# Performance work log

Measured on AMD Instinct MI355X. Metric: run time of the kernel, lower is better.

Reference implementation:

```python
import jax, jax.numpy as jnp
import numpy as np

EPS = 1e-5


def setup_inputs() -> dict:
    key = jax.random.key(0)
    ks = jax.random.split(key, 5)
    N, E, D, L = 10000, 160000, 512, 3
    x = jax.random.normal(ks[0], (N, D), dtype=jnp.float32)
    src = jax.random.randint(ks[1], (E,), 0, N, dtype=jnp.int64)
    dst = jax.random.randint(ks[2], (E,), 0, N, dtype=jnp.int64)
    gamma = jnp.ones((L, D), dtype=jnp.float32)
    beta = jnp.zeros((L, D), dtype=jnp.float32)
    # glorot-ish scale so ReLU stack stays well-conditioned
    W = jax.random.normal(ks[3], (L, D, D), dtype=jnp.float32) * (1.0 / np.sqrt(D))
    b = jnp.zeros((L, D), dtype=jnp.float32)
    return {"x": x, "src": src, "dst": dst, "gamma": gamma, "beta": beta, "W": W, "b": b}


def reference(x, src, dst, gamma, beta, W, b):
    N = x.shape[0]
    ones = jnp.ones(src.shape[0], dtype=x.dtype)
    # DGL GraphConv norm='both': src side uses out-degree, dst side uses in-degree
    out_deg = jnp.clip(jax.ops.segment_sum(ones, src, num_segments=N), 1.0)
    in_deg = jnp.clip(jax.ops.segment_sum(ones, dst, num_segments=N), 1.0)
    src_norm = (out_deg ** -0.5)[:, None]  # [N,1]
    dst_norm = (in_deg ** -0.5)[:, None]   # [N,1]
    n_layers = gamma.shape[0]
    for i in range(n_layers):
        # BatchNorm1d (training mode: batch mean, biased variance)
        mu = jnp.mean(x, axis=0)
        var = jnp.var(x, axis=0)
        x = (x - mu) * jax.lax.rsqrt(var + EPS) * gamma[i] + beta[i]
        h = x * src_norm
        agg = jax.ops.segment_sum(h[src], dst, num_segments=N) * dst_norm
        x = jax.nn.relu(agg @ W[i] + b[i])
    return x
```

## Files before the change

kernel.cpp:

```cpp
#include <hip/hip_runtime.h>
#include <hip/hip_bf16.h>

constexpr int N = 10000;
constexpr int D = 512;
constexpr int E = 160000;
constexpr int L = 3;
constexpr float EPS = 1e-5f;

constexpr int NSH = 4;
constexpr int SHC = D / NSH;

typedef _Float16 half8 __attribute__((ext_vector_type(8)));
typedef _Float16 half2v __attribute__((ext_vector_type(2)));
typedef float floatx4 __attribute__((ext_vector_type(4)));

__device__ __forceinline__ void glds16(const _Float16* g, _Float16* l) {
    __builtin_amdgcn_global_load_lds(
        (const __attribute__((address_space(1))) uint32_t*)(g),
        (__attribute__((address_space(3))) uint32_t*)(l),
        16, 0, 0);
}

constexpr int DEG_BLOCKS  = (E + 255) / 256;
constexpr int STAT_BLOCKS = 500;
constexpr int TW_BLOCKS   = L * 256;
constexpr int MEGA_BLOCKS = DEG_BLOCKS + STAT_BLOCKS + TW_BLOCKS;

__global__ __launch_bounds__(256) void mega_setup(
    const int* __restrict__ src, const int* __restrict__ dst,
    const float* __restrict__ x, const float* __restrict__ W,
    int* __restrict__ out_deg, int* __restrict__ in_deg,
    float* __restrict__ stats0, _Float16* __restrict__ Wt) {
    __shared__ float tb[32][33];
    int bid = blockIdx.x;
    int tid = threadIdx.x;
    if (bid < DEG_BLOCKS) {
        int e = bid * 256 + tid;
        if (e < E) {
            atomicAdd(&out_deg[src[e]], 1);
            atomicAdd(&in_deg[dst[e]], 1);
        }
    } else if (bid < DEG_BLOCKS + STAT_BLOCKS) {
        int b = bid - DEG_BLOCKS;
        int r0 = b * 20;
        int r1 = r0 + 20; if (r1 > N) r1 = N;
        int c2 = tid * 2;
        float s0 = 0.f, s1 = 0.f, q0 = 0.f, q1 = 0.f;
        for (int r = r0; r < r1; ++r) {
            float2 v = *(const float2*)(x + (size_t)r * D + c2);
            s0 += v.x; q0 += v.x * v.x;
            s1 += v.y; q1 += v.y * v.y;
        }
        atomicAdd(&stats0[c2], s0);
        atomicAdd(&stats0[c2 + 1], s1);
        atomicAdd(&stats0[D + c2], q0);
        atomicAdd(&stats0[D + c2 + 1], q1);
    } else {
        int b = bid - DEG_BLOCKS - STAT_BLOCKS;
        int l = b >> 8;
        int t = b & 255;
        int k0 = (t >> 4) * 32, n0 = (t & 15) * 32;
        int tx = tid & 31, ty = tid >> 5;
        const float* Wl = W + (size_t)l * D * D;
        _Float16* Wtl = Wt + (size_t)l * D * D;
        for (int i = 0; i < 32; i += 8)
            tb[ty + i][tx] = Wl[(size_t)(k0 + ty + i) * D + n0 + tx];
        __syncthreads();
        for (int i = 0; i < 32; i += 8)
            Wtl[(size_t)(n0 + ty + i) * D + k0 + tx] = (_Float16)tb[tx][ty + i];
    }
}

__global__ void scan_indeg(const int* __restrict__ in_deg,
                           const int* __restrict__ out_deg,
                           int* __restrict__ off, int* __restrict__ cursor,
                           float* __restrict__ src_norm, float* __restrict__ dst_norm) {
    __shared__ int lsum[1024];
    int t = threadIdx.x;
    const int chunk = (N + 1023) / 1024;
    int start = t * chunk;
    int end = start + chunk; if (end > N) end = N;
    int s = 0;
    for (int i = start; i < end; ++i) s += in_deg[i];
    lsum[t] = s;
    __syncthreads();
    for (int d = 1; d < 1024; d <<= 1) {
        int v = (t >= d) ? lsum[t - d] : 0;
        __syncthreads();
        lsum[t] += v;
        __syncthreads();
    }
    int excl = (t == 0) ? 0 : lsum[t - 1];
    for (int i = start; i < end; ++i) {
        off[i] = excl;
        cursor[i] = excl;
        excl += in_deg[i];
        int od = out_deg[i]; if (od < 1) od = 1;
        int id = in_deg[i];  if (id < 1) id = 1;
        src_norm[i] = rsqrtf((float)od);
        dst_norm[i] = rsqrtf((float)id);
    }
    if (t == 1023) off[N] = lsum[1023];
}

constexpr int CONV_BLOCKS = 500;
__global__ __launch_bounds__(256) void csr_fill_conv(
    const int* __restrict__ src, const int* __restrict__ dst,
    const float* __restrict__ x, const float* __restrict__ src_norm,
    int* __restrict__ cursor, int* __restrict__ csr_src,
    float* __restrict__ T, _Float16* __restrict__ x16) {
    int bid = blockIdx.x;
    int tid = threadIdx.x;
    if (bid < DEG_BLOCKS) {
        int e = bid * 256 + tid;
        if (e < E) {
            int s = src[e], d = dst[e];
            int pos = atomicAdd(&cursor[d], 1);
            csr_src[pos] = s;
            atomicAdd(&T[d], src_norm[s]);
        }
    } else {
        int b = bid - DEG_BLOCKS;
        int r0 = b * 20;
        int r1 = r0 + 20; if (r1 > N) r1 = N;
        int c2 = tid * 2;
        for (int r = r0; r < r1; ++r) {
            float sn = src_norm[r];
            float2 v = *(const float2*)(x + (size_t)r * D + c2);
            half2v h;
            h[0] = (_Float16)(v.x * sn);
            h[1] = (_Float16)(v.y * sn);
            *(half2v*)(x16 + (size_t)r * D + c2) = h;
        }
    }
}

__global__ __launch_bounds__(256) void aggregate4(
    const _Float16* __restrict__ xs, const int* __restrict__ off,
    const int* __restrict__ csr_src, const float* __restrict__ T,
    const float* __restrict__ dst_norm, const float* __restrict__ stats,
    const float* __restrict__ gamma, const float* __restrict__ beta,
    _Float16* __restrict__ agg) {
    int shard = blockIdx.x & 3;
    int wid = (blockIdx.x >> 2) * 4 + (threadIdx.x >> 6);
    int lane = threadIdx.x & 63;
    int eg = lane >> 4;
    int ch = lane & 15;
    int c0 = shard * SHC + ch * 8;

    int e0 = off[wid], e1 = off[wid + 1];
    const _Float16* xp = xs + c0;
    float a[8] = {}, b2[8] = {};
    int e = e0 + eg;
    for (; e + 4 < e1; e += 8) {
        int s0 = csr_src[e];
        int s1 = csr_src[e + 4];
        half8 v0 = *(const half8*)(xp + (size_t)s0 * D);
        half8 v1 = *(const half8*)(xp + (size_t)s1 * D);
#pragma unroll
        for (int k = 0; k < 8; ++k) { a[k] += (float)v0[k]; b2[k] += (float)v1[k]; }
    }
    if (e < e1) {
        int s0 = csr_src[e];
        half8 v0 = *(const half8*)(xp + (size_t)s0 * D);
#pragma unroll
        for (int k = 0; k < 8; ++k) a[k] += (float)v0[k];
    }
#pragma unroll
    for (int k = 0; k < 8; ++k) {
        a[k] += b2[k];
        a[k] += __shfl_xor(a[k], 16);
        a[k] += __shfl_xor(a[k], 32);
    }
    if (eg == 0) {
        float t = T[wid];
        float dn = dst_norm[wid];
        const float invN = 1.0f / (float)N;
        half8 o;
#pragma unroll
        for (int k = 0; k < 8; ++k) {
            int c = c0 + k;
            float mu = stats[c] * invN;
            float var = stats[D + c] * invN - mu * mu;
            float sc = gamma[c] * rsqrtf(var + EPS);
            float sh = beta[c] - mu * sc;
            o[k] = (_Float16)(dn * (sc * a[k] + sh * t));
        }
        *(half8*)(agg + (size_t)wid * D + c0) = o;
    }
}

template <typename OutT, bool STATS>
__global__ __launch_bounds__(256) void mm_f16_relu(
    const _Float16* __restrict__ A, const _Float16* __restrict__ Bt,
    const float* __restrict__ bias, OutT* __restrict__ C, int M,
    float* __restrict__ stats, const float* __restrict__ src_norm) {
    __shared__ __align__(16) _Float16 As[128 * 32];
    __shared__ __align__(16) _Float16 Bs[128 * 32];
    const int tid  = threadIdx.x;
    const int wave = tid >> 6;
    const int lane = tid & 63;
    const int quad = lane >> 4;
    const int l16  = lane & 15;
    const int row0 = blockIdx.x * 128;
    const int col0 = blockIdx.y * 128;
    const int wm = (wave & 1) * 64;
    const int wn = (wave >> 1) * 64;
    const int sr = lane >> 2;
    const int sc = (lane & 3) * 8;

    int ar0 = row0 + wave * 32 + sr;
    int ar1 = ar0 + 16;
    if (ar0 >= M) ar0 = M - 1;
    if (ar1 >= M) ar1 = M - 1;
    const _Float16* gA0 = A + (size_t)ar0 * D + sc;
    const _Float16* gA1 = A + (size_t)ar1 * D + sc;
    const _Float16* gB0 = Bt + (size_t)(col0 + wave * 32 + sr) * D + sc;
    const _Float16* gB1 = Bt + (size_t)(col0 + wave * 32 + 16 + sr) * D + sc;
    _Float16* lA0 = As + (wave * 32) * 32;
    _Float16* lA1 = As + (wave * 32 + 16) * 32;
    _Float16* lB0 = Bs + (wave * 32) * 32;
    _Float16* lB1 = Bs + (wave * 32 + 16) * 32;

    floatx4 acc[4][4] = {};

    for (int k0 = 0; k0 < D; k0 += 32) {
        __syncthreads();
        glds16(gA0 + k0, lA0);
        glds16(gA1 + k0, lA1);
        glds16(gB0 + k0, lB0);
        glds16(gB1 + k0, lB1);
        __syncthreads();
        half8 af[4], bf[4];
        for (int i = 0; i < 4; ++i)
            af[i] = *(const half8*)(As + (wm + i * 16 + l16) * 32 + quad * 8);
        for (int j = 0; j < 4; ++j)
            bf[j] = *(const half8*)(Bs + (wn + j * 16 + l16) * 32 + quad * 8);
        for (int i = 0; i < 4; ++i)
            for (int j = 0; j < 4; ++j)
                acc[i][j] = __builtin_amdgcn_mfma_f32_16x16x32_f16(
                    af[i], bf[j], acc[i][j], 0, 0, 0);
    }

    float s[4] = {}, q[4] = {};
    for (int i = 0; i < 4; ++i) {
        for (int r = 0; r < 4; ++r) {
            int row = row0 + wm + i * 16 + quad * 4 + r;
            bool valid = row < M;
            float sn = 1.0f;
            if (STATS && valid) sn = src_norm[row];
            for (int j = 0; j < 4; ++j) {
                int col = col0 + wn + j * 16 + l16;
                float v = acc[i][j][r] + bias[col];
                v = v > 0.f ? v : 0.f;
                if (valid) {
                    if (STATS) {
                        C[(size_t)row * D + col] = (OutT)(v * sn);
                        s[j] += v; q[j] += v * v;
                    } else {
                        C[(size_t)row * D + col] = (OutT)v;
                    }
                }
            }
        }
    }
    if (STATS) {
        for (int j = 0; j < 4; ++j) {
            float sv = s[j], qv = q[j];
            sv += __shfl_xor(sv, 16); sv += __shfl_xor(sv, 32);
            qv += __shfl_xor(qv, 16); qv += __shfl_xor(qv, 32);
            if (quad == 0) {
                int col = col0 + wn + j * 16 + l16;
                atomicAdd(&stats[col], sv);
                atomicAdd(&stats[D + col], qv);
            }
        }
    }
}

extern "C" void kernel_launch(void* const* d_in, const int* in_sizes, int n_in,
                              void* d_out, int out_size, void* d_ws, size_t ws_size,
                              hipStream_t stream) {
    const float* x_in  = (const float*)d_in[0];
    const int*   src   = (const int*)d_in[1];
    const int*   dst   = (const int*)d_in[2];
    const float* gamma = (const float*)d_in[3];
    const float* beta  = (const float*)d_in[4];
    const float* W     = (const float*)d_in[5];
    const float* b     = (const float*)d_in[6];
    float* out = (float*)d_out;

    char* p = (char*)d_ws;
    _Float16* x16 = (_Float16*)p;  p += (size_t)N * D * 2;
    _Float16* agg = (_Float16*)p;  p += (size_t)N * D * 2;
    _Float16* Wt  = (_Float16*)p;  p += (size_t)L * D * D * 2;
    float* src_norm = (float*)p;   p += (size_t)N * 4;
    float* dst_norm = (float*)p;   p += (size_t)N * 4;
    int* out_deg   = (int*)p;      p += (size_t)N * 4;
    int* in_deg    = (int*)p;      p += (size_t)N * 4;
    float* stats0  = (float*)p;    p += 2 * D * 4;
    float* stats1  = (float*)p;    p += 2 * D * 4;
    float* stats2  = (float*)p;    p += 2 * D * 4;
    float* T       = (float*)p;    p += (size_t)N * 4;
    int* csr_off   = (int*)p;      p += (size_t)(N + 1) * 4;
    int* cursor    = (int*)p;      p += (size_t)N * 4;
    int* csr_src   = (int*)p;      p += (size_t)E * 4;

    float* stats_in[3] = {stats0, stats1, stats2};

    hipMemsetAsync(out_deg, 0, (3 * (size_t)N + 6 * D) * sizeof(int), stream);
    mega_setup<<<MEGA_BLOCKS, 256, 0, stream>>>(src, dst, x_in, W,
                                                out_deg, in_deg, stats0, Wt);
    scan_indeg<<<1, 1024, 0, stream>>>(in_deg, out_deg, csr_off, cursor,
                                       src_norm, dst_norm);
    csr_fill_conv<<<DEG_BLOCKS + CONV_BLOCKS, 256, 0, stream>>>(
        src, dst, x_in, src_norm, cursor, csr_src, T, x16);

    dim3 mm_grid((N + 127) / 128, D / 128);
    const int agg_blocks = NSH * ((N + 3) / 4);

    for (int l = 0; l < L; ++l) {
        const float* gl  = gamma + (size_t)l * D;
        const float* bl  = beta + (size_t)l * D;
        const _Float16* Wl = Wt + (size_t)l * D * D;
        const float* bil = b + (size_t)l * D;

        aggregate4<<<agg_blocks, 256, 0, stream>>>(
            x16, csr_off, csr_src, T, dst_norm, stats_in[l], gl, bl, agg);
        if (l == L - 1) {
            mm_f16_relu<float, false><<<mm_grid, 256, 0, stream>>>(
                agg, Wl, bil, out, N, nullptr, nullptr);
        } else {
            mm_f16_relu<_Float16, true><<<mm_grid, 256, 0, stream>>>(
                agg, Wl, bil, x16, N, stats_in[l + 1], src_norm);
        }
    }
}
```

Measured before the change: 321.1 us.

## Assign one wave per node over all channels in aggregation, unroll edges by six

```diff
diff --git a/kernel.cpp b/kernel.cpp
--- a/kernel.cpp
+++ b/kernel.cpp
@@ -6,9 +6,6 @@
 constexpr int E = 160000;
 constexpr int L = 3;
 constexpr float EPS = 1e-5f;
-
-constexpr int NSH = 4;
-constexpr int SHC = D / NSH;
 
 typedef _Float16 half8 __attribute__((ext_vector_type(8)));
 typedef _Float16 half2v __attribute__((ext_vector_type(2)));
@@ -135,59 +132,62 @@
     }
 }
 
-__global__ __launch_bounds__(256) void aggregate4(
+__global__ __launch_bounds__(256) void aggregate_pre(
     const _Float16* __restrict__ xs, const int* __restrict__ off,
     const int* __restrict__ csr_src, const float* __restrict__ T,
     const float* __restrict__ dst_norm, const float* __restrict__ stats,
     const float* __restrict__ gamma, const float* __restrict__ beta,
     _Float16* __restrict__ agg) {
-    int shard = blockIdx.x & 3;
-    int wid = (blockIdx.x >> 2) * 4 + (threadIdx.x >> 6);
+    int wid = blockIdx.x * 4 + (threadIdx.x >> 6);
     int lane = threadIdx.x & 63;
-    int eg = lane >> 4;
-    int ch = lane & 15;
-    int c0 = shard * SHC + ch * 8;
-
-    int e0 = off[wid], e1 = off[wid + 1];
+    int c0 = lane * 8;
     const _Float16* xp = xs + c0;
+
+    int e0 = __builtin_amdgcn_readfirstlane(off[wid]);
+    int e1 = __builtin_amdgcn_readfirstlane(off[wid + 1]);
+
     float a[8] = {}, b2[8] = {};
-    int e = e0 + eg;
-    for (; e + 4 < e1; e += 8) {
+    int e = e0;
+    for (; e + 6 <= e1; e += 6) {
         int s0 = csr_src[e];
-        int s1 = csr_src[e + 4];
+        int s1 = csr_src[e + 1];
+        int s2 = csr_src[e + 2];
+        int s3 = csr_src[e + 3];
+        int s4 = csr_src[e + 4];
+        int s5 = csr_src[e + 5];
         half8 v0 = *(const half8*)(xp + (size_t)s0 * D);
         half8 v1 = *(const half8*)(xp + (size_t)s1 * D);
+        half8 v2 = *(const half8*)(xp + (size_t)s2 * D);
+        half8 v3 = *(const half8*)(xp + (size_t)s3 * D);
+        half8 v4 = *(const half8*)(xp + (size_t)s4 * D);
+        half8 v5 = *(const half8*)(xp + (size_t)s5 * D);
 #pragma unroll
-        for (int k = 0; k < 8; ++k) { a[k] += (float)v0[k]; b2[k] += (float)v1[k]; }
-    }
-    if (e < e1) {
+        for (int k = 0; k < 8; ++k) {
+            a[k]  += (float)v0[k] + (float)v2[k] + (float)v4[k];
+            b2[k] += (float)v1[k] + (float)v3[k] + (float)v5[k];
+        }
+    }
+    for (; e < e1; ++e) {
         int s0 = csr_src[e];
         half8 v0 = *(const half8*)(xp + (size_t)s0 * D);
 #pragma unroll
         for (int k = 0; k < 8; ++k) a[k] += (float)v0[k];
     }
+
+    float t = T[wid];
+    float dn = dst_norm[wid];
+    const float invN = 1.0f / (float)N;
+    half8 o;
 #pragma unroll
     for (int k = 0; k < 8; ++k) {
-        a[k] += b2[k];
-        a[k] += __shfl_xor(a[k], 16);
-        a[k] += __shfl_xor(a[k], 32);
-    }
-    if (eg == 0) {
-        float t = T[wid];
-        float dn = dst_norm[wid];
-        const float invN = 1.0f / (float)N;
-        half8 o;
-#pragma unroll
-        for (int k = 0; k < 8; ++k) {
-            int c = c0 + k;
-            float mu = stats[c] * invN;
-            float var = stats[D + c] * invN - mu * mu;
-            float sc = gamma[c] * rsqrtf(var + EPS);
-            float sh = beta[c] - mu * sc;
-            o[k] = (_Float16)(dn * (sc * a[k] + sh * t));
-        }
-        *(half8*)(agg + (size_t)wid * D + c0) = o;
-    }
+        int c = c0 + k;
+        float mu = stats[c] * invN;
+        float var = stats[D + c] * invN - mu * mu;
+        float sc = gamma[c] * rsqrtf(var + EPS);
+        float sh = beta[c] - mu * sc;
+        o[k] = (_Float16)(dn * (sc * (a[k] + b2[k]) + sh * t));
+    }
+    *(half8*)(agg + (size_t)wid * D + c0) = o;
 }
 
 template <typename OutT, bool STATS>
@@ -317,7 +317,7 @@
         src, dst, x_in, src_norm, cursor, csr_src, T, x16);
 
     dim3 mm_grid((N + 127) / 128, D / 128);
-    const int agg_blocks = NSH * ((N + 3) / 4);
+    const int agg_blocks = (N + 3) / 4;
 
     for (int l = 0; l < L; ++l) {
         const float* gl  = gamma + (size_t)l * D;
@@ -325,7 +325,7 @@
         const _Float16* Wl = Wt + (size_t)l * D * D;
         const float* bil = b + (size_t)l * D;
 
-        aggregate4<<<agg_blocks, 256, 0, stream>>>(
+        aggregate_pre<<<agg_blocks, 256, 0, stream>>>(
             x16, csr_off, csr_src, T, dst_norm, stats_in[l], gl, bl, agg);
         if (l == L - 1) {
             mm_f16_relu<float, false><<<mm_grid, 256, 0, stream>>>(
```

New measurement: 302.9 us. -5.6%, faster.
